# Optimization experiments

Measured on AMD Instinct MI355X. Metric: run time of the kernel, lower is better.

The kernel has to match this reference:

```python
import jax, jax.numpy as jnp
import numpy as np

EPS = 1e-5

def _neighbor_idx(H, W):
    # flat index of the 3x3 clamped neighborhood for each pixel, [H*W, 9]
    r = np.arange(H)[:, None, None]  # [H,1,1]
    c = np.arange(W)[None, :, None]  # [1,W,1]
    dr = np.repeat(np.array([-1, 0, 1]), 3)[None, None, :]  # [1,1,9]
    dc = np.tile(np.array([-1, 0, 1]), 3)[None, None, :]
    ri = np.clip(r + dr, 0, H - 1)
    ci = np.clip(c + dc, 0, W - 1)
    return jnp.asarray((ri * W + ci).reshape(H * W, 9))

def setup_inputs() -> dict:
    key = jax.random.key(0)
    ks = jax.random.split(key, 7)
    B, C, H, W = 16, 256, 80, 80
    s = 1.0 / np.sqrt(C)
    return {
        "x": jax.random.normal(ks[0], (B, C, H, W), jnp.float32),
        "Wq": jax.random.normal(ks[1], (C, C), jnp.float32) * s,
        "bq": jax.random.normal(ks[2], (C,), jnp.float32) * s,
        "Wk": jax.random.normal(ks[3], (C, C), jnp.float32) * s,
        "bk": jax.random.normal(ks[4], (C,), jnp.float32) * s,
        "Wv": jax.random.normal(ks[5], (C, C), jnp.float32) * s,
        "bv": jax.random.normal(ks[6], (C,), jnp.float32) * s,
    }

def reference(x, Wq, bq, Wk, bk, Wv, bv):
    B, C, H, W = x.shape
    N = H * W
    xf = x.reshape(B, C, N)
    # 1x1 convs as channel GEMMs
    q = jnp.einsum('oc,bcn->bno', Wq, xf) + bq          # [B,N,C]
    k = jnp.einsum('oc,bcn->bon', Wk, xf) + bk[:, None]  # [B,C,N]
    v = jnp.einsum('oc,bcn->bon', Wv, xf) + bv[:, None]  # [B,C,N]
    idx = _neighbor_idx(H, W)                            # [N,9]
    k_n = k[:, :, idx]                                   # [B,C,N,9]
    v_n = v[:, :, idx]                                   # [B,C,N,9]
    # raw attention scores (NOT softmaxed before AV, matching the source)
    scores = jnp.einsum('bnc,bcnq->bnq', q, k_n)         # [B,N,9]
    new_v = jnp.einsum('bnq,bcnq->bcn', scores, v_n).reshape(B, C, H, W)
    out9 = scores.reshape(B, H, W, 9)
    center = out9[..., 4]
    others_mean = (out9.sum(-1) - center) / 8.0
    output = jnp.stack([center, others_mean], axis=-1)   # [B,H,W,2]
    # residual + layer_norm over [H,W] (no affine), per (B,C)
    xr = x + new_v
    mu = xr.mean(axis=(-2, -1), keepdims=True)
    var = ((xr - mu) ** 2).mean(axis=(-2, -1), keepdims=True)
    x_out = (xr - mu) * jax.lax.rsqrt(var + EPS)
    return (output, x_out)
```

## Files before the change

### kernel.cpp

```cpp
#include <hip/hip_runtime.h>
#include <hip/hip_bf16.h>

using f32x4  = __attribute__((ext_vector_type(4))) float;
using short8 = __attribute__((ext_vector_type(8))) short;
using bf16   = __hip_bfloat16;

constexpr int BATCH = 16;
constexpr int CH    = 256;
constexpr int HH    = 80;
constexpr int WW    = 80;
constexpr int NPIX  = HH * WW;

__device__ __forceinline__ float b2f(unsigned short u) {
    union { unsigned int i; float f; } x;
    x.i = ((unsigned int)u) << 16;
    return x.f;
}

__global__ __launch_bounds__(256) void convert_w(
    const float* __restrict__ Wq, const float* __restrict__ Wk,
    const float* __restrict__ Wv, bf16* __restrict__ Wb)
{
    const int elem = blockIdx.x * 256 + threadIdx.x;
    const int mat  = blockIdx.y;
    const float* src = (mat == 0) ? Wq : (mat == 1) ? Wk : Wv;
    Wb[(size_t)mat * CH * CH + elem] = __float2bfloat16(src[elem]);
}

__global__ __launch_bounds__(256) void transpose_cast(
    const float* __restrict__ x, bf16* __restrict__ xt, int b0)
{
    __shared__ float t[64][65];
    const int b  = b0 + blockIdx.z;
    const int n0 = blockIdx.x * 64;
    const int c0 = blockIdx.y * 64;
    const float* xb = x + (size_t)b * CH * NPIX;
    const int tid = threadIdx.x;

    {
        const int nl  = tid & 63;
        const int cl0 = tid >> 6;
        #pragma unroll
        for (int i = 0; i < 16; ++i) {
            const int cl = cl0 + i * 4;
            t[cl][nl] = xb[(size_t)(c0 + cl) * NPIX + n0 + nl];
        }
    }
    __syncthreads();
    {
        bf16* xtb = xt + (size_t)blockIdx.z * NPIX * CH;
        const int cl  = tid & 63;
        const int nl0 = tid >> 6;
        #pragma unroll
        for (int i = 0; i < 16; ++i) {
            const int nl = nl0 + i * 4;
            xtb[(size_t)(n0 + nl) * CH + c0 + cl] = __float2bfloat16(t[cl][nl]);
        }
    }
}

__global__ __launch_bounds__(256) void qkv_mfma(
    const bf16* __restrict__ xt, const bf16* __restrict__ Wb,
    const float* __restrict__ bq, const float* __restrict__ bk,
    const float* __restrict__ bv,
    bf16* __restrict__ qo, bf16* __restrict__ ko, bf16* __restrict__ vt)
{
    const int m  = blockIdx.z % 3;
    const int bl = blockIdx.z / 3;
    const int n0 = blockIdx.x * 128;
    const int o0 = blockIdx.y * 128;
    const bf16*  W    = Wb + (size_t)m * CH * CH;
    const float* bias = (m == 0) ? bq : (m == 1) ? bk : bv;
    const bf16*  A    = xt + (size_t)bl * NPIX * CH;

    __shared__ short As[128 * 36];
    __shared__ short Bs[128 * 36];

    const int tid = threadIdx.x;
    const int wv  = tid >> 6, ln = tid & 63;
    const int wr  = wv >> 1,  wc = wv & 1;
    const int lm  = ln & 15,  lk = ln >> 4;

    f32x4 acc[4][4];
    #pragma unroll
    for (int i = 0; i < 4; ++i)
        #pragma unroll
        for (int j = 0; j < 4; ++j)
            #pragma unroll
            for (int r = 0; r < 4; ++r) acc[i][j][r] = 0.f;

    for (int k0 = 0; k0 < CH; k0 += 32) {
        #pragma unroll
        for (int it = 0; it < 2; ++it) {
            const int q   = tid + it * 256;
            const int row = q >> 2, ch = q & 3;
            const int4 av = *(const int4*)(A + (size_t)(n0 + row) * CH + k0 + ch * 8);
            *(int4*)((char*)As + row * 72 + ch * 16) = av;
            const int4 wvv = *(const int4*)(W + (size_t)(o0 + row) * CH + k0 + ch * 8);
            *(int4*)((char*)Bs + row * 72 + ch * 16) = wvv;
        }
        __syncthreads();

        short8 afr[4], bfr[4];
        #pragma unroll
        for (int i = 0; i < 4; ++i) {
            const int row = wr * 64 + i * 16 + lm;
            afr[i] = *(const short8*)((const char*)As + row * 72 + lk * 16);
        }
        #pragma unroll
        for (int j = 0; j < 4; ++j) {
            const int row = wc * 64 + j * 16 + lm;
            bfr[j] = *(const short8*)((const char*)Bs + row * 72 + lk * 16);
        }
        if (m < 2) {
            #pragma unroll
            for (int i = 0; i < 4; ++i)
                #pragma unroll
                for (int j = 0; j < 4; ++j)
                    acc[i][j] = __builtin_amdgcn_mfma_f32_16x16x32_bf16(
                        bfr[j], afr[i], acc[i][j], 0, 0, 0);
        } else {
            #pragma unroll
            for (int i = 0; i < 4; ++i)
                #pragma unroll
                for (int j = 0; j < 4; ++j)
                    acc[i][j] = __builtin_amdgcn_mfma_f32_16x16x32_bf16(
                        afr[i], bfr[j], acc[i][j], 0, 0, 0);
        }
        __syncthreads();
    }

    if (m < 2) {
        bf16* out = (m == 0 ? qo : ko) + (size_t)bl * NPIX * CH;
        #pragma unroll
        for (int j = 0; j < 4; ++j) {
            const int ob = o0 + wc * 64 + j * 16 + lk * 4;
            const float4 b4 = *(const float4*)(bias + ob);
            #pragma unroll
            for (int i = 0; i < 4; ++i) {
                const int n = n0 + wr * 64 + i * 16 + lm;
                ushort4 pk;
                {
                    const bf16 h0 = __float2bfloat16(acc[i][j][0] + b4.x);
                    const bf16 h1 = __float2bfloat16(acc[i][j][1] + b4.y);
                    const bf16 h2 = __float2bfloat16(acc[i][j][2] + b4.z);
                    const bf16 h3 = __float2bfloat16(acc[i][j][3] + b4.w);
                    pk.x = *(const unsigned short*)&h0;
                    pk.y = *(const unsigned short*)&h1;
                    pk.z = *(const unsigned short*)&h2;
                    pk.w = *(const unsigned short*)&h3;
                }
                *(ushort4*)(out + (size_t)n * CH + ob) = pk;
            }
        }
    } else {
        bf16* out = vt + (size_t)bl * CH * NPIX;
        #pragma unroll
        for (int j = 0; j < 4; ++j) {
            const int o = o0 + wc * 64 + j * 16 + lm;
            const float bs = bias[o];
            #pragma unroll
            for (int i = 0; i < 4; ++i) {
                const int nb = n0 + wr * 64 + i * 16 + lk * 4;
                ushort4 pk;
                #pragma unroll
                for (int r = 0; r < 4; ++r) {
                    const bf16 h = __float2bfloat16(acc[i][j][r] + bs);
                    ((unsigned short*)&pk)[r] = *(const unsigned short*)&h;
                }
                *(ushort4*)(out + (size_t)o * NPIX + nb) = pk;
            }
        }
    }
}

__global__ __launch_bounds__(256) void scores_kernel(
    const bf16* __restrict__ q, const bf16* __restrict__ k,
    float* __restrict__ scores, float* __restrict__ out0, int b0)
{
    const int wave = threadIdx.x >> 6, lane = threadIdx.x & 63;
    const int n  = blockIdx.x * 4 + wave;
    const int bl = blockIdx.y;
    const int b  = b0 + bl;

    const unsigned short* qrow = (const unsigned short*)(q + ((size_t)bl * NPIX + n) * CH) + lane * 4;
    const unsigned short* kb   = (const unsigned short*)(k + (size_t)bl * NPIX * CH);

    const ushort4 qu = *(const ushort4*)qrow;
    const float q0 = b2f(qu.x), q1 = b2f(qu.y), q2 = b2f(qu.z), q3 = b2f(qu.w);

    const int r = n / WW, col = n % WW;
    float s[9], ssum = 0.f;
    #pragma unroll
    for (int j = 0; j < 9; ++j) {
        const int rr = min(max(r + j / 3 - 1, 0), HH - 1);
        const int c2 = min(max(col + j % 3 - 1, 0), WW - 1);
        const int nbr = rr * WW + c2;
        const ushort4 kv = *(const ushort4*)(kb + (size_t)nbr * CH + lane * 4);
        float d = q0 * b2f(kv.x) + q1 * b2f(kv.y) + q2 * b2f(kv.z) + q3 * b2f(kv.w);
        #pragma unroll
        for (int off = 32; off >= 1; off >>= 1) d += __shfl_xor(d, off, 64);
        s[j] = d;
        ssum += d;
    }
    if (lane == 0) {
        float* sp = scores + (size_t)bl * 9 * NPIX;
        #pragma unroll
        for (int j = 0; j < 9; ++j) sp[(size_t)j * NPIX + n] = s[j];
        const float center = s[4];
        out0[((size_t)b * NPIX + n) * 2 + 0] = center;
        out0[((size_t)b * NPIX + n) * 2 + 1] = (ssum - center) * 0.125f;
    }
}

__global__ __launch_bounds__(320) void newv_ln(
    const float* __restrict__ x, const bf16* __restrict__ vt,
    const float* __restrict__ scores, float* __restrict__ xout, int b0)
{
    __shared__ __align__(16) unsigned short lds_v[NPIX];
    __shared__ float rsum[5], rsq[5];

    const int c  = blockIdx.x;
    const int bl = blockIdx.y;
    const int b  = b0 + bl;
    const int tid = threadIdx.x;

    const unsigned short* vrow = (const unsigned short*)(vt + ((size_t)bl * CH + c) * NPIX);
    const float* xrow = x + ((size_t)b * CH + c) * NPIX;
    const float* sb   = scores + (size_t)bl * 9 * NPIX;

    #pragma unroll
    for (int i = 0; i < 3; ++i) {
        const int t = tid + i * 320;
        if (t < NPIX / 8) ((int4*)lds_v)[t] = ((const int4*)vrow)[t];
    }
    __syncthreads();

    float val[20];
    float sum = 0.f, sq = 0.f;
    #pragma unroll
    for (int it = 0; it < 5; ++it) {
        const int p   = tid + it * 320;
        const int n0  = p * 4;
        const int r   = p / 20;
        const int c0  = (p % 20) * 4;

        const int rm = max(r - 1, 0) * WW;
        const int r0 = r * WW;
        const int rp = min(r + 1, HH - 1) * WW;

        float4 s[9];
        #pragma unroll
        for (int j = 0; j < 9; ++j)
            s[j] = *(const float4*)(sb + (size_t)j * NPIX + n0);

        const float4 xin = *(const float4*)(xrow + n0);

        const int cA = max(c0 - 1, 0);
        const int cF = min(c0 + 4, WW - 1);
        float vm[6], v0[6], vp[6];
        vm[0] = b2f(lds_v[rm + cA]); v0[0] = b2f(lds_v[r0 + cA]); vp[0] = b2f(lds_v[rp + cA]);
        #pragma unroll
        for (int t = 1; t < 5; ++t) {
            vm[t] = b2f(lds_v[rm + c0 + t - 1]);
            v0[t] = b2f(lds_v[r0 + c0 + t - 1]);
            vp[t] = b2f(lds_v[rp + c0 + t - 1]);
        }
        vm[5] = b2f(lds_v[rm + cF]); v0[5] = b2f(lds_v[r0 + cF]); vp[5] = b2f(lds_v[rp + cF]);

        #pragma unroll
        for (int px = 0; px < 4; ++px) {
            const float sc0 = ((const float*)&s[0])[px];
            const float sc1 = ((const float*)&s[1])[px];
            const float sc2 = ((const float*)&s[2])[px];
            const float sc3 = ((const float*)&s[3])[px];
            const float sc4 = ((const float*)&s[4])[px];
            const float sc5 = ((const float*)&s[5])[px];
            const float sc6 = ((const float*)&s[6])[px];
            const float sc7 = ((const float*)&s[7])[px];
            const float sc8 = ((const float*)&s[8])[px];
            float a;
            a  = sc0 * vm[px] + sc1 * vm[px + 1] + sc2 * vm[px + 2];
            a += sc3 * v0[px] + sc4 * v0[px + 1] + sc5 * v0[px + 2];
            a += sc6 * vp[px] + sc7 * vp[px + 1] + sc8 * vp[px + 2];
            const float vv = ((const float*)&xin)[px] + a;
            val[it * 4 + px] = vv;
            sum += vv;
            sq  += vv * vv;
        }
    }

    #pragma unroll
    for (int off = 32; off >= 1; off >>= 1) {
        sum += __shfl_xor(sum, off, 64);
        sq  += __shfl_xor(sq,  off, 64);
    }
    const int wave = tid >> 6, lane = tid & 63;
    if (lane == 0) { rsum[wave] = sum; rsq[wave] = sq; }
    __syncthreads();
    sum = rsum[0] + rsum[1] + rsum[2] + rsum[3] + rsum[4];
    sq  = rsq[0]  + rsq[1]  + rsq[2]  + rsq[3]  + rsq[4];

    const float mu   = sum * (1.f / NPIX);
    const float var  = sq * (1.f / NPIX) - mu * mu;
    const float rstd = rsqrtf(var + 1e-5f);

    float* orow = xout + ((size_t)b * CH + c) * NPIX;
    #pragma unroll
    for (int it = 0; it < 5; ++it) {
        const int n0 = (tid + it * 320) * 4;
        float4 o;
        o.x = (val[it * 4 + 0] - mu) * rstd;
        o.y = (val[it * 4 + 1] - mu) * rstd;
        o.z = (val[it * 4 + 2] - mu) * rstd;
        o.w = (val[it * 4 + 3] - mu) * rstd;
        *(float4*)(orow + n0) = o;
    }
}

extern "C" void kernel_launch(void* const* d_in, const int* in_sizes, int n_in,
                              void* d_out, int out_size, void* d_ws, size_t ws_size,
                              hipStream_t stream)
{
    const float* x  = (const float*)d_in[0];
    const float* Wq = (const float*)d_in[1];
    const float* bq = (const float*)d_in[2];
    const float* Wk = (const float*)d_in[3];
    const float* bk = (const float*)d_in[4];
    const float* Wv = (const float*)d_in[5];
    const float* bv = (const float*)d_in[6];

    float* out0 = (float*)d_out;
    float* xout = out0 + (size_t)BATCH * NPIX * 2;

    char* ws = (char*)d_ws;
    bf16* Wb = (bf16*)ws;
    ws += (size_t)3 * CH * CH * sizeof(bf16);

    const size_t fBF = (size_t)NPIX * CH * sizeof(bf16);
    const size_t fSC = (size_t)NPIX * 9 * sizeof(float);
    const size_t perBatch = 4 * fBF + fSC;

    size_t avail = ws_size - ((size_t)3 * CH * CH * sizeof(bf16));
    int NB = (int)(avail / perBatch);
    if (NB < 1)  NB = 1;
    if (NB > BATCH) NB = BATCH;

    bf16*  xt  = (bf16*)ws;
    bf16*  qb  = (bf16*)(ws + (size_t)NB * fBF);
    bf16*  kb  = (bf16*)(ws + (size_t)NB * fBF * 2);
    bf16*  vt  = (bf16*)(ws + (size_t)NB * fBF * 3);
    float* sc  = (float*)(ws + (size_t)NB * fBF * 4);

    convert_w<<<dim3(CH * CH / 256, 3), 256, 0, stream>>>(Wq, Wk, Wv, Wb);

    for (int b0 = 0; b0 < BATCH; b0 += NB) {
        const int cnb = (BATCH - b0 < NB) ? (BATCH - b0) : NB;

        transpose_cast<<<dim3(NPIX / 64, CH / 64, cnb), 256, 0, stream>>>(x, xt, b0);

        qkv_mfma<<<dim3(NPIX / 128, CH / 128, cnb * 3), 256, 0, stream>>>(
            xt, Wb, bq, bk, bv, qb, kb, vt);

        scores_kernel<<<dim3(NPIX / 4, cnb), 256, 0, stream>>>(qb, kb, sc, out0, b0);

        newv_ln<<<dim3(CH, cnb), 320, 0, stream>>>(x, vt, sc, xout, b0);
    }
}
```

Before: 326.7 us.

## Double-buffer QKV GEMM LDS tiles with async global-to-LDS loads and XOR swizzle

The QKV MFMA GEMM now stages its A and W tiles straight into LDS with global_load_lds, skipping the trip through registers. Two LDS buffers let the next k-step load while the current one computes, which also removes one barrier per iteration. The padded row layout becomes an XOR-swizzled 64-byte layout to avoid bank conflicts, and launch bounds now request 4 blocks per CU. The risks are correctness if load-to-LDS completion is not properly waited before the barrier, and register pressure from the occupancy hint.

```diff
diff --git a/kernel.cpp b/kernel.cpp
--- a/kernel.cpp
+++ b/kernel.cpp
@@ -15,6 +15,14 @@
     union { unsigned int i; float f; } x;
     x.i = ((unsigned int)u) << 16;
     return x.f;
+}
+
+typedef __attribute__((address_space(3))) void  lds_void;
+typedef __attribute__((address_space(1))) const void glb_void;
+__device__ __forceinline__ void glds16(const void* g, void* l) {
+    __builtin_amdgcn_global_load_lds((glb_void*)(unsigned long long)g,
+                                     (lds_void*)(unsigned int)(unsigned long long)l,
+                                     16, 0, 0);
 }
 
 __global__ __launch_bounds__(256) void convert_w(
@@ -59,7 +67,7 @@
     }
 }
 
-__global__ __launch_bounds__(256) void qkv_mfma(
+__global__ __launch_bounds__(256, 4) void qkv_mfma(
     const bf16* __restrict__ xt, const bf16* __restrict__ Wb,
     const float* __restrict__ bq, const float* __restrict__ bk,
     const float* __restrict__ bv,
@@ -73,8 +81,8 @@
     const float* bias = (m == 0) ? bq : (m == 1) ? bk : bv;
     const bf16*  A    = xt + (size_t)bl * NPIX * CH;
 
-    __shared__ short As[128 * 36];
-    __shared__ short Bs[128 * 36];
+    __shared__ char As[2][128 * 64];
+    __shared__ char Bs[2][128 * 64];
 
     const int tid = threadIdx.x;
     const int wv  = tid >> 6, ln = tid & 63;
@@ -89,28 +97,37 @@
             #pragma unroll
             for (int r = 0; r < 4; ++r) acc[i][j][r] = 0.f;
 
-    for (int k0 = 0; k0 < CH; k0 += 32) {
+    auto stage = [&](int buf, int k0) {
         #pragma unroll
         for (int it = 0; it < 2; ++it) {
-            const int q   = tid + it * 256;
-            const int row = q >> 2, ch = q & 3;
-            const int4 av = *(const int4*)(A + (size_t)(n0 + row) * CH + k0 + ch * 8);
-            *(int4*)((char*)As + row * 72 + ch * 16) = av;
-            const int4 wvv = *(const int4*)(W + (size_t)(o0 + row) * CH + k0 + ch * 8);
-            *(int4*)((char*)Bs + row * 72 + ch * 16) = wvv;
-        }
+            const int idx = it * 256 + tid;
+            const int row = idx >> 2;
+            const int pos = idx & 3;
+            const int chk = pos ^ ((row >> 1) & 3);
+            glds16(A + (size_t)(n0 + row) * CH + k0 + chk * 8, &As[buf][idx * 16]);
+            glds16(W + (size_t)(o0 + row) * CH + k0 + chk * 8, &Bs[buf][idx * 16]);
+        }
+    };
+
+    stage(0, 0);
+    int buf = 0;
+    #pragma unroll
+    for (int t = 0; t < 8; ++t) {
         __syncthreads();
+        if (t < 7) stage(buf ^ 1, (t + 1) * 32);
 
         short8 afr[4], bfr[4];
         #pragma unroll
         for (int i = 0; i < 4; ++i) {
             const int row = wr * 64 + i * 16 + lm;
-            afr[i] = *(const short8*)((const char*)As + row * 72 + lk * 16);
+            const int chk = lk ^ ((row >> 1) & 3);
+            afr[i] = *(const short8*)&As[buf][row * 64 + chk * 16];
         }
         #pragma unroll
         for (int j = 0; j < 4; ++j) {
             const int row = wc * 64 + j * 16 + lm;
-            bfr[j] = *(const short8*)((const char*)Bs + row * 72 + lk * 16);
+            const int chk = lk ^ ((row >> 1) & 3);
+            bfr[j] = *(const short8*)&Bs[buf][row * 64 + chk * 16];
         }
         if (m < 2) {
             #pragma unroll
@@ -127,7 +144,7 @@
                     acc[i][j] = __builtin_amdgcn_mfma_f32_16x16x32_bf16(
                         afr[i], bfr[j], acc[i][j], 0, 0, 0);
         }
-        __syncthreads();
+        buf ^= 1;
     }
 
     if (m < 2) {
```

Measured after the change: 575.5 us. 1.76x slower.
